# Optimization experiments

Measured on AMD Instinct MI355X. Metric: run time of the kernel, lower is better.

## Reference

```python
import jax, jax.numpy as jnp
import numpy as np

VOCAB = 50257
D = 1024
EDGES = [0, 20000, 40000, VOCAB]  # cluster boundaries
HSZ = [1024, 256, 64]             # D // 4**i per cluster


def setup_inputs() -> dict:
    key = jax.random.key(0)
    ks = jax.random.split(key, 8)
    emb_input = jax.random.randint(ks[0], (8, 2048), 0, VOCAB, dtype=jnp.int64)
    inp = {"emb_input": emb_input}
    for i in range(3):
        vsz = EDGES[i + 1] - EDGES[i]
        h = HSZ[i]
        inp[f"emb{i}"] = jax.random.normal(ks[1 + 2 * i], (vsz, h), dtype=jnp.float32) * 0.02
        # nn.Linear(h, D, bias=False) weight has shape [D, h]
        inp[f"w{i}"] = jax.random.normal(ks[2 + 2 * i], (D, h), dtype=jnp.float32) * 0.02
    return inp


def reference(emb_input, emb0, w0, emb1, w1, emb2, w2):
    B, S = emb_input.shape
    idx = emb_input.reshape(-1)  # [N]
    clusters = [(emb0, w0), (emb1, w1), (emb2, w2)]
    out = jnp.zeros((idx.shape[0], D), dtype=jnp.float32)
    for i, (emb, w) in enumerate(clusters):
        lo, hi = EDGES[i], EDGES[i + 1]
        mask = (idx >= lo) & (idx < hi)                       # [N]
        local = jnp.clip(idx - lo, 0, emb.shape[0] - 1)       # in-range gather ids
        h = emb[local]                                        # [N, hsz_i]
        proj = jnp.einsum('nh,dh->nd', h, w)                  # [N, D]
        out = out + jnp.where(mask[:, None], proj, 0.0)
    return out.reshape(B, S, D)
```

## Files before the change

kernel.cpp:

```cpp
#include <hip/hip_runtime.h>
#include <hip/hip_bf16.h>
#include <stdint.h>

#define DOUT 1024
#define NMAX 16384

#define BM 256
#define BN 128
#define LDSBUF 49152
#define BOFFS 32768

typedef __attribute__((ext_vector_type(8))) short short8;
typedef __attribute__((ext_vector_type(4))) float floatx4;

__device__ __forceinline__ unsigned short f2bf(float f) {
  union { float f; uint32_t u; } v;
  v.f = f;
  return (unsigned short)((v.u + 0x7FFFu + ((v.u >> 16) & 1u)) >> 16);
}

__device__ __forceinline__ ushort4 cvt4(float4 v) {
  __hip_bfloat162 p0 = __float22bfloat162_rn(make_float2(v.x, v.y));
  __hip_bfloat162 p1 = __float22bfloat162_rn(make_float2(v.z, v.w));
  union { __hip_bfloat162 h[2]; ushort4 s; } u;
  u.h[0] = p0; u.h[1] = p1;
  return u.s;
}

__global__ __launch_bounds__(256) void classify_cvt_kernel(
    const int* __restrict__ idx, int* __restrict__ cnt,
    int* __restrict__ bucket, int* __restrict__ blocal, int N,
    const float* __restrict__ w0, const float* __restrict__ w1,
    const float* __restrict__ w2, unsigned short* __restrict__ wb0,
    unsigned short* __restrict__ wb1, unsigned short* __restrict__ wb2) {
  if (blockIdx.x < 64) {
    int n = blockIdx.x * 256 + threadIdx.x;
    int lane = threadIdx.x & 63;
    int c = -1, v = 0;
    if (n < N) {
      v = idx[n];
      c = (v < 20000) ? 0 : ((v < 40000) ? 1 : 2);
    }
#pragma unroll
    for (int k = 0; k < 3; ++k) {
      unsigned long long m = __ballot(c == k);
      if (c == k) {
        int leader = __ffsll((unsigned long long)m) - 1;
        int base = 0;
        if (lane == leader) base = atomicAdd(&cnt[k], (int)__popcll(m));
        base = __shfl(base, leader);
        int rank = (int)__popcll(m & ((1ull << (unsigned)lane) - 1ull));
        int lo = (k == 0) ? 0 : (k == 1) ? 20000 : 40000;
        bucket[k * NMAX + base + rank] = n;
        blocal[k * NMAX + base + rank] = v - lo;
      }
    }
  } else {
    int i = (blockIdx.x - 64) * 256 + threadIdx.x;
    if (i >= 344064) return;
    const float4* src;
    ushort4* dst;
    if (i < 262144) {
      src = (const float4*)w0 + i;
      dst = (ushort4*)wb0 + i;
    } else if (i < 327680) {
      src = (const float4*)w1 + (i - 262144);
      dst = (ushort4*)wb1 + (i - 262144);
    } else {
      src = (const float4*)w2 + (i - 327680);
      dst = (ushort4*)wb2 + (i - 327680);
    }
    float4 v = *src;
    ushort4 o;
    o.x = f2bf(v.x); o.y = f2bf(v.y); o.z = f2bf(v.z); o.w = f2bf(v.w);
    *dst = o;
  }
}

__global__ __launch_bounds__(256) void gather_kernel(
    const float* __restrict__ emb0, const float* __restrict__ emb1,
    const float* __restrict__ emb2, const int* __restrict__ cnt,
    const int* __restrict__ blocal, unsigned short* __restrict__ Abf) {
  const int b = blockIdx.x;
  const int c0 = cnt[0], c1 = cnt[1], c2 = cnt[2];
  const float* emb;
  const int* bl;
  int H, count, baseRow, lg;
  size_t off;
  if (b < 4096) {
    emb = emb0; bl = blocal; H = 1024; count = c0; off = 0;
    baseRow = b * 4; lg = 6;
  } else if (b < 5120) {
    emb = emb1; bl = blocal + NMAX; H = 256; count = c1;
    off = (size_t)c0 * 1024; baseRow = (b - 4096) * 16; lg = 4;
  } else {
    emb = emb2; bl = blocal + 2 * NMAX; H = 64; count = c2;
    off = (size_t)c0 * 1024 + (size_t)c1 * 256; baseRow = (b - 5120) * 64; lg = 2;
  }
  const int tid = threadIdx.x;
  const int r = baseRow + (tid >> lg);
  if (r >= count) return;
  const int tpr = 1 << lg;
  const int e = (tid & (tpr - 1)) * 4;
  const int stride = tpr * 4;
  const float* src = emb + (size_t)bl[r] * H + e;
  unsigned short* d = Abf + off + (size_t)r * H + e;
#pragma unroll
  for (int j = 0; j < 4; ++j) {
    float4 v = *(const float4*)(src + j * stride);
    *(ushort4*)(d + j * stride) = cvt4(v);
  }
}

template <int H>
__device__ __forceinline__ void tile_compute(
    const unsigned short* __restrict__ A, const unsigned short* __restrict__ B,
    int count, const int* __restrict__ bucket, float* __restrict__ out,
    char* lds, int* rowTok, int by, int bx) {
  constexpr int NT = H / 64;
  const int m0 = by * BM;
  const int n0 = bx * BN;

  const int tid = threadIdx.x;
  const int wave = tid >> 6;
  const int lane = tid & 63;
  const int quad = lane >> 4;
  const int l16 = lane & 15;
  const int wm = wave & 3;
  const int wn = wave >> 2;

  if (tid < BM) {
    int m = m0 + tid;
    rowTok[tid] = (m < count) ? bucket[m] : -1;
  }

  const int dl = wave * 1024 + lane * 16;
  const int lswz = dl ^ (((dl >> 7) & 3) << 4);
  const int rW = lswz >> 6;
  const int ckW = (lswz >> 4) & 3;
  const char* Abyte = (const char*)A;
  const char* Bbyte = (const char*)B;
  const size_t aOff0 = ((size_t)(m0 + rW) * H) * 2 + ckW * 16;
  const size_t aOff1 = ((size_t)(m0 + 128 + rW) * H) * 2 + ckW * 16;
  const size_t bOff = ((size_t)(n0 + rW) * H) * 2 + ckW * 16;

  auto stage = [&](int kt, char* buf) {
    const int kb = kt * 128;
#pragma unroll
    for (int s = 0; s < 2; ++s) {
      __builtin_amdgcn_global_load_lds(
          (const __attribute__((address_space(1))) void*)(Abyte + aOff0 + kb + s * 64),
          (__attribute__((address_space(3))) void*)(buf + s * 16384 + wave * 1024),
          16, 0, 0);
      __builtin_amdgcn_global_load_lds(
          (const __attribute__((address_space(1))) void*)(Abyte + aOff1 + kb + s * 64),
          (__attribute__((address_space(3))) void*)(buf + s * 16384 + 8192 + wave * 1024),
          16, 0, 0);
      __builtin_amdgcn_global_load_lds(
          (const __attribute__((address_space(1))) void*)(Bbyte + bOff + kb + s * 64),
          (__attribute__((address_space(3))) void*)(buf + BOFFS + s * 8192 + wave * 1024),
          16, 0, 0);
    }
  };

  int offA[2][4], offB[2][4];
#pragma unroll
  for (int s = 0; s < 2; ++s) {
#pragma unroll
    for (int i = 0; i < 4; ++i) {
      int ba = (wm * 64 + i * 16 + l16) * 64 + quad * 16;
      offA[s][i] = s * 16384 + (ba ^ (((ba >> 7) & 3) << 4));
      int bb = (wn * 64 + i * 16 + l16) * 64 + quad * 16;
      offB[s][i] = BOFFS + s * 8192 + (bb ^ (((bb >> 7) & 3) << 4));
    }
  }

  if (NT >= 1) stage(0, lds);
  if (NT >= 2) stage(1, lds + LDSBUF);
  if (NT >= 3) stage(2, lds + 2 * LDSBUF);

  floatx4 acc[4][4];
#pragma unroll
  for (int i = 0; i < 4; ++i)
#pragma unroll
    for (int j = 0; j < 4; ++j) acc[i][j] = (floatx4){0.f, 0.f, 0.f, 0.f};

#pragma unroll
  for (int kt = 0; kt < NT; ++kt) {
    const int rem = NT - 1 - kt;
    if (rem >= 2)
      asm volatile("s_waitcnt vmcnt(12)" ::: "memory");
    else if (rem == 1)
      asm volatile("s_waitcnt vmcnt(6)" ::: "memory");
    else
      asm volatile("s_waitcnt vmcnt(0)" ::: "memory");
    asm volatile("s_barrier" ::: "memory");

    const char* buf = lds + (kt % 3) * LDSBUF;
    short8 a[2][4], b[2][4];
#pragma unroll
    for (int s = 0; s < 2; ++s)
#pragma unroll
      for (int i = 0; i < 4; ++i) {
        a[s][i] = *(const short8*)(buf + offA[s][i]);
        b[s][i] = *(const short8*)(buf + offB[s][i]);
      }
    __builtin_amdgcn_s_setprio(1);
#pragma unroll
    for (int s = 0; s < 2; ++s)
#pragma unroll
      for (int i = 0; i < 4; ++i)
#pragma unroll
        for (int j = 0; j < 4; ++j)
          acc[i][j] = __builtin_amdgcn_mfma_f32_16x16x32_bf16(
              a[s][i], b[s][j], acc[i][j], 0, 0, 0);
    __builtin_amdgcn_s_setprio(0);
    asm volatile("s_barrier" ::: "memory");
    if (kt + 3 < NT) stage(kt + 3, lds + (kt % 3) * LDSBUF);
  }

  const int colBase = n0 + wn * 64 + l16;
#pragma unroll
  for (int mi = 0; mi < 4; ++mi) {
#pragma unroll
    for (int r = 0; r < 4; ++r) {
      int tok = rowTok[wm * 64 + mi * 16 + quad * 4 + r];
      if (tok >= 0) {
        float* o = out + (size_t)tok * DOUT + colBase;
#pragma unroll
        for (int ni = 0; ni < 4; ++ni) o[ni * 16] = acc[mi][ni][r];
      }
    }
  }
}

__global__ __launch_bounds__(512) void gemm_persist(
    const unsigned short* __restrict__ Abf,
    const unsigned short* __restrict__ wb0,
    const unsigned short* __restrict__ wb1,
    const unsigned short* __restrict__ wb2, const int* __restrict__ cnt,
    const int* __restrict__ bucket, float* __restrict__ out,
    int* __restrict__ tileCtr) {
  __shared__ __align__(16) char lds[3 * LDSBUF + BM * 4 + 16];
  int* rowTok = (int*)(lds + 3 * LDSBUF);
  int* curTile = (int*)(lds + 3 * LDSBUF + BM * 4);

  const int c0 = cnt[0], c1 = cnt[1], c2 = cnt[2];
  const int nt0 = (c0 + BM - 1) / BM;
  const int nt1 = (c1 + BM - 1) / BM;
  const int nt2 = (c2 + BM - 1) / BM;
  const int T0 = nt0 * 8, T1 = nt1 * 8, T2 = nt2 * 8;
  const int total = T0 + T1 + T2;
  const size_t o1 = (size_t)c0 * 1024;
  const size_t o2 = o1 + (size_t)c1 * 256;

  for (;;) {
    __syncthreads();
    if (threadIdx.x == 0) *curTile = atomicAdd(tileCtr, 1);
    __syncthreads();
    const int t = *curTile;
    if (t >= total) return;
    if (t < T0) {
      tile_compute<1024>(Abf, wb0, c0, bucket, out, lds, rowTok, t >> 3, t & 7);
    } else if (t < T0 + T1) {
      const int u = t - T0;
      tile_compute<256>(Abf + o1, wb1, c1, bucket + NMAX, out, lds, rowTok,
                        u >> 3, u & 7);
    } else {
      const int u = t - T0 - T1;
      tile_compute<64>(Abf + o2, wb2, c2, bucket + 2 * NMAX, out, lds, rowTok,
                       u >> 3, u & 7);
    }
  }
}

extern "C" void kernel_launch(void* const* d_in, const int* in_sizes, int n_in,
                              void* d_out, int out_size, void* d_ws, size_t ws_size,
                              hipStream_t stream) {
  const int* idx = (const int*)d_in[0];
  const float* emb0 = (const float*)d_in[1];
  const float* w0 = (const float*)d_in[2];
  const float* emb1 = (const float*)d_in[3];
  const float* w1 = (const float*)d_in[4];
  const float* emb2 = (const float*)d_in[5];
  const float* w2 = (const float*)d_in[6];
  float* out = (float*)d_out;
  const int N = in_sizes[0];

  char* ws = (char*)d_ws;
  int* cnt = (int*)ws;
  int* bucket = (int*)(ws + 1024);
  int* blocal = bucket + 3 * NMAX;
  size_t off = 1024 + (size_t)6 * NMAX * 4;
  off = (off + 255) & ~(size_t)255;
  unsigned short* wb0 = (unsigned short*)(ws + off); off += (size_t)DOUT * 1024 * 2;
  unsigned short* wb1 = (unsigned short*)(ws + off); off += (size_t)DOUT * 256 * 2;
  unsigned short* wb2 = (unsigned short*)(ws + off); off += (size_t)DOUT * 64 * 2;
  off = (off + 255) & ~(size_t)255;
  unsigned short* Abf = (unsigned short*)(ws + off);
  off += (size_t)(NMAX + 256) * 1024 * 2;

  hipMemsetAsync(cnt, 0, 16 * sizeof(int), stream);

  classify_cvt_kernel<<<64 + 1344, 256, 0, stream>>>(
      idx, cnt, bucket, blocal, N, w0, w1, w2, wb0, wb1, wb2);

  gather_kernel<<<5376, 256, 0, stream>>>(emb0, emb1, emb2, cnt, blocal, Abf);

  gemm_persist<<<256, 512, 0, stream>>>(Abf, wb0, wb1, wb2, cnt, bucket, out,
                                        cnt + 8);
}
```

Baseline: 198.5 us.

## Halve K-tile to shrink LDS and run two persistent GEMM blocks per CU

The K step per stage drops from 128 to 64 elements, which halves each LDS buffer (three buffers now total about 74KB instead of 147KB). The main loop becomes a non-unrolled rotating triple-buffer with an explicit tail, and the H=64 cluster gets a two-stage special case. Launch bounds ask for higher occupancy and the persistent grid doubles to 512 blocks, so two 512-thread blocks can share a CU and hide latency. The cost is twice as many barriers and waits per unit of K, and possible register pressure from the tighter launch bound.

```diff
diff --git a/kernel.cpp b/kernel.cpp
--- a/kernel.cpp
+++ b/kernel.cpp
@@ -7,8 +7,8 @@
 
 #define BM 256
 #define BN 128
-#define LDSBUF 49152
-#define BOFFS 32768
+#define LDSBUF 24576
+#define BOFFS 16384
 
 typedef __attribute__((ext_vector_type(8))) short short8;
 typedef __attribute__((ext_vector_type(4))) float floatx4;
@@ -117,7 +117,7 @@
     const unsigned short* __restrict__ A, const unsigned short* __restrict__ B,
     int count, const int* __restrict__ bucket, float* __restrict__ out,
     char* lds, int* rowTok, int by, int bx) {
-  constexpr int NT = H / 64;
+  constexpr int NT = H / 32;
   const int m0 = by * BM;
   const int n0 = bx * BN;
 
@@ -136,87 +136,94 @@
 
   const int dl = wave * 1024 + lane * 16;
   const int lswz = dl ^ (((dl >> 7) & 3) << 4);
-  const int rW = lswz >> 6;
-  const int ckW = (lswz >> 4) & 3;
+  const int rA = lswz >> 6;
+  const int ck = (lswz >> 4) & 3;
   const char* Abyte = (const char*)A;
   const char* Bbyte = (const char*)B;
-  const size_t aOff0 = ((size_t)(m0 + rW) * H) * 2 + ckW * 16;
-  const size_t aOff1 = ((size_t)(m0 + 128 + rW) * H) * 2 + ckW * 16;
-  const size_t bOff = ((size_t)(n0 + rW) * H) * 2 + ckW * 16;
+  const size_t aSrc0 = ((size_t)(m0 + rA) * H) * 2 + ck * 16;
+  const size_t aSrc1 = ((size_t)(m0 + 128 + rA) * H) * 2 + ck * 16;
+  const size_t bSrc = ((size_t)(n0 + rA) * H) * 2 + ck * 16;
 
   auto stage = [&](int kt, char* buf) {
-    const int kb = kt * 128;
-#pragma unroll
-    for (int s = 0; s < 2; ++s) {
-      __builtin_amdgcn_global_load_lds(
-          (const __attribute__((address_space(1))) void*)(Abyte + aOff0 + kb + s * 64),
-          (__attribute__((address_space(3))) void*)(buf + s * 16384 + wave * 1024),
-          16, 0, 0);
-      __builtin_amdgcn_global_load_lds(
-          (const __attribute__((address_space(1))) void*)(Abyte + aOff1 + kb + s * 64),
-          (__attribute__((address_space(3))) void*)(buf + s * 16384 + 8192 + wave * 1024),
-          16, 0, 0);
-      __builtin_amdgcn_global_load_lds(
-          (const __attribute__((address_space(1))) void*)(Bbyte + bOff + kb + s * 64),
-          (__attribute__((address_space(3))) void*)(buf + BOFFS + s * 8192 + wave * 1024),
-          16, 0, 0);
-    }
+    const size_t kb = (size_t)kt * 64;
+    __builtin_amdgcn_global_load_lds(
+        (const __attribute__((address_space(1))) void*)(Abyte + aSrc0 + kb),
+        (__attribute__((address_space(3))) void*)(buf + wave * 1024), 16, 0, 0);
+    __builtin_amdgcn_global_load_lds(
+        (const __attribute__((address_space(1))) void*)(Abyte + aSrc1 + kb),
+        (__attribute__((address_space(3))) void*)(buf + 8192 + wave * 1024), 16, 0, 0);
+    __builtin_amdgcn_global_load_lds(
+        (const __attribute__((address_space(1))) void*)(Bbyte + bSrc + kb),
+        (__attribute__((address_space(3))) void*)(buf + BOFFS + wave * 1024), 16, 0, 0);
   };
 
-  int offA[2][4], offB[2][4];
-#pragma unroll
-  for (int s = 0; s < 2; ++s) {
+  int offA[4], offB[4];
+#pragma unroll
+  for (int i = 0; i < 4; ++i) {
+    int ba = (wm * 64 + i * 16 + l16) * 64 + quad * 16;
+    offA[i] = ba ^ (((ba >> 7) & 3) << 4);
+    int bb = (wn * 64 + i * 16 + l16) * 64 + quad * 16;
+    offB[i] = BOFFS + (bb ^ (((bb >> 7) & 3) << 4));
+  }
+
+  floatx4 acc[4][4];
+#pragma unroll
+  for (int i = 0; i < 4; ++i)
+#pragma unroll
+    for (int j = 0; j < 4; ++j) acc[i][j] = (floatx4){0.f, 0.f, 0.f, 0.f};
+
+  auto compute = [&](const char* buf) {
+    short8 a[4], b[4];
 #pragma unroll
     for (int i = 0; i < 4; ++i) {
-      int ba = (wm * 64 + i * 16 + l16) * 64 + quad * 16;
-      offA[s][i] = s * 16384 + (ba ^ (((ba >> 7) & 3) << 4));
-      int bb = (wn * 64 + i * 16 + l16) * 64 + quad * 16;
-      offB[s][i] = BOFFS + s * 8192 + (bb ^ (((bb >> 7) & 3) << 4));
-    }
-  }
-
-  if (NT >= 1) stage(0, lds);
-  if (NT >= 2) stage(1, lds + LDSBUF);
-  if (NT >= 3) stage(2, lds + 2 * LDSBUF);
-
-  floatx4 acc[4][4];
-#pragma unroll
-  for (int i = 0; i < 4; ++i)
-#pragma unroll
-    for (int j = 0; j < 4; ++j) acc[i][j] = (floatx4){0.f, 0.f, 0.f, 0.f};
-
-#pragma unroll
-  for (int kt = 0; kt < NT; ++kt) {
-    const int rem = NT - 1 - kt;
-    if (rem >= 2)
-      asm volatile("s_waitcnt vmcnt(12)" ::: "memory");
-    else if (rem == 1)
+      a[i] = *(const short8*)(buf + offA[i]);
+      b[i] = *(const short8*)(buf + offB[i]);
+    }
+    __builtin_amdgcn_s_setprio(1);
+#pragma unroll
+    for (int i = 0; i < 4; ++i)
+#pragma unroll
+      for (int j = 0; j < 4; ++j)
+        acc[i][j] = __builtin_amdgcn_mfma_f32_16x16x32_bf16(
+            a[i], b[j], acc[i][j], 0, 0, 0);
+    __builtin_amdgcn_s_setprio(0);
+  };
+
+  if constexpr (NT >= 3) {
+    stage(0, lds);
+    stage(1, lds + LDSBUF);
+    stage(2, lds + 2 * LDSBUF);
+    char* b0 = lds;
+    char* b1 = lds + LDSBUF;
+    char* b2 = lds + 2 * LDSBUF;
+#pragma unroll 1
+    for (int kt = 0; kt < NT - 3; ++kt) {
       asm volatile("s_waitcnt vmcnt(6)" ::: "memory");
-    else
-      asm volatile("s_waitcnt vmcnt(0)" ::: "memory");
-    asm volatile("s_barrier" ::: "memory");
-
-    const char* buf = lds + (kt % 3) * LDSBUF;
-    short8 a[2][4], b[2][4];
-#pragma unroll
-    for (int s = 0; s < 2; ++s)
-#pragma unroll
-      for (int i = 0; i < 4; ++i) {
-        a[s][i] = *(const short8*)(buf + offA[s][i]);
-        b[s][i] = *(const short8*)(buf + offB[s][i]);
-      }
-    __builtin_amdgcn_s_setprio(1);
-#pragma unroll
-    for (int s = 0; s < 2; ++s)
-#pragma unroll
-      for (int i = 0; i < 4; ++i)
-#pragma unroll
-        for (int j = 0; j < 4; ++j)
-          acc[i][j] = __builtin_amdgcn_mfma_f32_16x16x32_bf16(
-              a[s][i], b[s][j], acc[i][j], 0, 0, 0);
-    __builtin_amdgcn_s_setprio(0);
-    asm volatile("s_barrier" ::: "memory");
-    if (kt + 3 < NT) stage(kt + 3, lds + (kt % 3) * LDSBUF);
+      asm volatile("s_barrier" ::: "memory");
+      compute(b0);
+      asm volatile("s_waitcnt lgkmcnt(0)" ::: "memory");
+      asm volatile("s_barrier" ::: "memory");
+      stage(kt + 3, b0);
+      char* t = b0; b0 = b1; b1 = b2; b2 = t;
+    }
+    asm volatile("s_waitcnt vmcnt(6)" ::: "memory");
+    asm volatile("s_barrier" ::: "memory");
+    compute(b0);
+    asm volatile("s_waitcnt vmcnt(3)" ::: "memory");
+    asm volatile("s_barrier" ::: "memory");
+    compute(b1);
+    asm volatile("s_waitcnt vmcnt(0)" ::: "memory");
+    asm volatile("s_barrier" ::: "memory");
+    compute(b2);
+  } else {
+    stage(0, lds);
+    stage(1, lds + LDSBUF);
+    asm volatile("s_waitcnt vmcnt(3)" ::: "memory");
+    asm volatile("s_barrier" ::: "memory");
+    compute(lds);
+    asm volatile("s_waitcnt vmcnt(0)" ::: "memory");
+    asm volatile("s_barrier" ::: "memory");
+    compute(lds + LDSBUF);
   }
 
   const int colBase = n0 + wn * 64 + l16;
@@ -234,7 +241,7 @@
   }
 }
 
-__global__ __launch_bounds__(512) void gemm_persist(
+__global__ __launch_bounds__(512, 4) void gemm_persist(
     const unsigned short* __restrict__ Abf,
     const unsigned short* __restrict__ wb0,
     const unsigned short* __restrict__ wb1,
@@ -307,6 +314,6 @@
 
   gather_kernel<<<5376, 256, 0, stream>>>(emb0, emb1, emb2, cnt, blocal, Abf);
 
-  gemm_persist<<<256, 512, 0, stream>>>(Abf, wb0, wb1, wb2, cnt, bucket, out,
+  gemm_persist<<<512, 512, 0, stream>>>(Abf, wb0, wb1, wb2, cnt, bucket, out,
                                         cnt + 8);
 }
```

New measurement: 201.4 us. About the same (+1.5%).
